# Performance work log

Hardware: AMD Instinct MI355X
Metric: run time of the kernel (lower is better)

## Reference

```python
import jax, jax.numpy as jnp
import numpy as np

B, N, D = 8, 2048, 512
S = 4096  # max_swaps


def setup_inputs() -> dict:
    key = jax.random.key(0)
    ks = jax.random.split(key, 5)
    h = jax.random.normal(ks[0], (B, N, D), dtype=jnp.float32)
    indices = jax.random.randint(ks[1], (B, S, 4), 0, N, dtype=jnp.int64)
    # MLP params (Linear stores weight as (out,in) in torch; we keep (in,out) and matmul)
    W1 = jax.random.normal(ks[2], (4 * D, D), dtype=jnp.float32) * (1.0 / np.sqrt(4 * D))
    b1 = jnp.zeros((D,), dtype=jnp.float32)
    W2 = jax.random.normal(ks[3], (D, D // 2), dtype=jnp.float32) * (1.0 / np.sqrt(D))
    b2 = jnp.zeros((D // 2,), dtype=jnp.float32)
    W3 = jax.random.normal(ks[4], (D // 2, 1), dtype=jnp.float32) * (1.0 / np.sqrt(D // 2))
    b3 = jnp.zeros((1,), dtype=jnp.float32)
    return {"h": h, "indices": indices, "W1": W1, "b1": b1, "W2": W2, "b2": b2, "W3": W3, "b3": b3}


def reference(h, indices, W1, b1, W2, b2, W3, b3):
    # h: (B, N, D); indices: (B, S, 4) node ids per swap
    swap_emb = jnp.take_along_axis(h[:, None, :, :], indices[..., None].astype(jnp.int32),
                                   axis=2)  # broadcast-gather -> (B, S, 4, D)
    # equivalently: h[batch_idx, indices]; implemented as per-batch gather
    swap_emb = jax.vmap(lambda hb, ib: hb[ib])(h, indices)  # (B, S, 4, D)
    swap_feats = swap_emb.reshape(h.shape[0], indices.shape[1], -1)  # (B, S, 4D)
    x = jax.nn.gelu(swap_feats @ W1 + b1, approximate=False)
    x = jax.nn.gelu(x @ W2 + b2, approximate=False)
    scores = (x @ W3 + b3)[..., 0]  # (B, S)
    rates = jax.nn.softplus(scores)
    return rates
```

## Files before the change

### kernel.cpp

```cpp
#include <hip/hip_runtime.h>
#include <math.h>

#define BATCH 8
#define NNODES 2048
#define DDIM 512
#define SWAPS 4096
#define M_TOTAL (BATCH * SWAPS)
#define KD DDIM
#define ND (4 * DDIM)
#define K2 DDIM
#define N2 (DDIM / 2)

typedef __attribute__((ext_vector_type(8))) __bf16 bf16x8;
typedef __attribute__((ext_vector_type(4))) float f32x4;
typedef __attribute__((ext_vector_type(8))) unsigned short us8;
typedef unsigned short ushort_t;

__device__ __forceinline__ float gelu_exact(float x) {
    return 0.5f * x * (1.0f + erff(x * 0.70710678118654752440f));
}
__device__ __forceinline__ float softplus_f(float x) {
    return fmaxf(x, 0.0f) + log1pf(expf(-fabsf(x)));
}
__device__ __forceinline__ unsigned short f2bf(float f) {
    unsigned int u = __builtin_bit_cast(unsigned int, f);
    u += 0x7FFFu + ((u >> 16) & 1u);
    return (unsigned short)(u >> 16);
}
__device__ __forceinline__ float bf2f(unsigned short s) {
    return __builtin_bit_cast(float, (unsigned int)s << 16);
}
__device__ __forceinline__ void glds16(const void* g, void* l) {
    __builtin_amdgcn_global_load_lds(
        (const __attribute__((address_space(1))) void*)g,
        (__attribute__((address_space(3))) void*)l, 16, 0, 0);
}

__global__ __launch_bounds__(256) void convert_kernel(
    const float* __restrict__ h, const float* __restrict__ W1,
    const float* __restrict__ W2, ushort_t* __restrict__ h_bf,
    ushort_t* __restrict__ W1pt, ushort_t* __restrict__ W2t)
{
    const int bid = blockIdx.x;
    if (bid < 8192) {
        size_t i = ((size_t)bid * 256 + threadIdx.x) * 4;
        float4 v = *(const float4*)(h + i);
        ushort4 o = { f2bf(v.x), f2bf(v.y), f2bf(v.z), f2bf(v.w) };
        *(ushort4*)(h_bf + i) = o;
    } else if (bid < 8192 + 1024) {
        size_t e = ((size_t)(bid - 8192) * 256 + threadIdx.x) * 4;
        const int k = (int)(e >> 9), n = (int)(e & 511);
        const int sg = k >> 9, d = k & 511;
        const int j = sg * 512 + n;
        float4 v = *(const float4*)(W1 + e);
        W1pt[(size_t)(j + 0) * KD + d] = f2bf(v.x);
        W1pt[(size_t)(j + 1) * KD + d] = f2bf(v.y);
        W1pt[(size_t)(j + 2) * KD + d] = f2bf(v.z);
        W1pt[(size_t)(j + 3) * KD + d] = f2bf(v.w);
    } else {
        size_t e = ((size_t)(bid - 9216) * 256 + threadIdx.x) * 4;
        const int k = (int)(e >> 8), n = (int)(e & 255);
        float4 v = *(const float4*)(W2 + e);
        W2t[(size_t)(n + 0) * K2 + k] = f2bf(v.x);
        W2t[(size_t)(n + 1) * K2 + k] = f2bf(v.y);
        W2t[(size_t)(n + 2) * K2 + k] = f2bf(v.z);
        W2t[(size_t)(n + 3) * K2 + k] = f2bf(v.w);
    }
}

__global__ __launch_bounds__(256) void gemm1_dense(
    const ushort_t* __restrict__ h_bf, const ushort_t* __restrict__ W1pt,
    ushort_t* __restrict__ P2)
{
    __shared__ __align__(16) char smem[32768];

    const int tid = threadIdx.x;
    const int w = tid >> 6, lane = tid & 63;
    const int quad = lane >> 4, l16 = lane & 15;
    const int wr = w >> 1, wc = w & 1;

    const int bid = blockIdx.x;
    const int xcd = bid & 7;
    const int r = bid >> 3;
    const int m0 = xcd * NNODES + (r & 15) * 128;
    const int n0 = (r >> 4) * 128;

    const int row0 = tid >> 2, sub = tid & 3;
    const int cg = (sub - (row0 >> 1)) & 3;
    const ushort_t* bA0 = h_bf + (size_t)(m0 + row0) * KD + cg * 8;
    const ushort_t* bA1 = h_bf + (size_t)(m0 + row0 + 64) * KD + cg * 8;
    const ushort_t* bB0 = W1pt + (size_t)(n0 + row0) * KD + cg * 8;
    const ushort_t* bB1 = W1pt + (size_t)(n0 + row0 + 64) * KD + cg * 8;

    int pa[4], pb[4];
    #pragma unroll
    for (int i = 0; i < 4; ++i) {
        const int rA = wr * 64 + i * 16 + l16;
        const int rB = wc * 64 + i * 16 + l16;
        pa[i] = rA * 64 + (((quad + (rA >> 1)) & 3) * 16);
        pb[i] = 8192 + rB * 64 + (((quad + (rB >> 1)) & 3) * 16);
    }

    f32x4 acc[4][4] = {};

    auto stage = [&](int kt, int half) {
        const int oo = kt * 32;
        char* base = smem + half * 16384;
        glds16(bA0 + oo, base + w * 1024);
        glds16(bA1 + oo, base + 4096 + w * 1024);
        glds16(bB0 + oo, base + 8192 + w * 1024);
        glds16(bB1 + oo, base + 12288 + w * 1024);
    };
    auto compute = [&](int half) {
        const char* base = smem + half * 16384;
        bf16x8 af[4], bfr[4];
        #pragma unroll
        for (int i = 0; i < 4; ++i) {
            af[i]  = *(const bf16x8*)(base + pa[i]);
            bfr[i] = *(const bf16x8*)(base + pb[i]);
        }
        #pragma unroll
        for (int i = 0; i < 4; ++i)
            #pragma unroll
            for (int jj = 0; jj < 4; ++jj)
                acc[i][jj] = __builtin_amdgcn_mfma_f32_16x16x32_bf16(
                    af[i], bfr[jj], acc[i][jj], 0, 0, 0);
    };

    for (int kt = 0; kt < 16; kt += 2) {
        stage(kt, 0);
        stage(kt + 1, 1);
        __syncthreads();
        compute(0);
        compute(1);
        __syncthreads();
    }

    #pragma unroll
    for (int jj = 0; jj < 4; ++jj) {
        const int j = n0 + wc * 64 + jj * 16 + l16;
        const int sg = j >> 9, nh = j & 511;
        const size_t base = ((size_t)(xcd * 2 + (nh >> 8)) * NNODES) * 1024
                          + (size_t)(sg << 8) + (nh & 255);
        #pragma unroll
        for (int i = 0; i < 4; ++i) {
            f32x4 v = acc[i][jj];
            #pragma unroll
            for (int rr = 0; rr < 4; ++rr) {
                const int node = (m0 + wr * 64 + i * 16 + quad * 4 + rr) & (NNODES - 1);
                P2[base + (size_t)node * 1024] = f2bf(v[rr]);
            }
        }
    }
}

__global__ __launch_bounds__(256) void gather_sum_kernel(
    const ushort_t* __restrict__ P2, const int* __restrict__ idx,
    const float* __restrict__ b1, ushort_t* __restrict__ x1_bf)
{
    const int bid = blockIdx.x;
    const int b = bid & 7;
    const int t = bid >> 3;
    const int nc = t >> 9;
    const int rg = t & 511;
    const int wave = threadIdx.x >> 6, lane = threadIdx.x & 63;
    const int rsel = lane >> 5, li = lane & 31;
    const int m = b * SWAPS + rg * 8 + wave * 2 + rsel;
    const int4 iv = *(const int4*)(idx + (size_t)m * 4);
    const ushort_t* Pr = P2 + ((size_t)(b * 2 + nc) * NNODES) * 1024;
    const int col = li * 8;

    float s[8];
    {
        const float* bp = b1 + nc * 256 + col;
        float4 ba = *(const float4*)bp;
        float4 bb = *(const float4*)(bp + 4);
        s[0] = ba.x; s[1] = ba.y; s[2] = ba.z; s[3] = ba.w;
        s[4] = bb.x; s[5] = bb.y; s[6] = bb.z; s[7] = bb.w;
    }
    const int nodes[4] = { iv.x, iv.y, iv.z, iv.w };
    #pragma unroll
    for (int sg = 0; sg < 4; ++sg) {
        us8 v = *(const us8*)(Pr + (size_t)nodes[sg] * 1024 + sg * 256 + col);
        #pragma unroll
        for (int u = 0; u < 8; ++u) s[u] += bf2f(v[u]);
    }
    us8 o;
    #pragma unroll
    for (int u = 0; u < 8; ++u)
        o[u] = f2bf(gelu_exact(s[u]));
    __builtin_nontemporal_store(o, (us8*)(x1_bf + (size_t)m * K2 + nc * 256 + col));
}

__global__ __launch_bounds__(256) void gemm2_partial(
    const ushort_t* __restrict__ x1_bf, const ushort_t* __restrict__ W2t,
    const float* __restrict__ b2, const float* __restrict__ W3,
    float* __restrict__ pp)
{
    __shared__ __align__(16) char smem[32768];

    const int tid = threadIdx.x;
    const int w = tid >> 6, lane = tid & 63;
    const int quad = lane >> 4, l16 = lane & 15;
    const int wr = w >> 1, wc = w & 1;
    const int m0 = blockIdx.y * 128, n0 = blockIdx.x * 128;

    const int row0 = tid >> 2, sub = tid & 3;
    const int cg = (sub - (row0 >> 1)) & 3;
    const ushort_t* bA0 = x1_bf + (size_t)(m0 + row0) * K2 + cg * 8;
    const ushort_t* bA1 = x1_bf + (size_t)(m0 + row0 + 64) * K2 + cg * 8;
    const ushort_t* bB0 = W2t + (size_t)(n0 + row0) * K2 + cg * 8;
    const ushort_t* bB1 = W2t + (size_t)(n0 + row0 + 64) * K2 + cg * 8;

    int pa[4], pb[4];
    #pragma unroll
    for (int i = 0; i < 4; ++i) {
        const int rA = wr * 64 + i * 16 + l16;
        const int rB = wc * 64 + i * 16 + l16;
        pa[i] = rA * 64 + (((quad + (rA >> 1)) & 3) * 16);
        pb[i] = 8192 + rB * 64 + (((quad + (rB >> 1)) & 3) * 16);
    }

    f32x4 acc[4][4] = {};

    auto stage = [&](int kt, int half) {
        const int oo = kt * 32;
        char* base = smem + half * 16384;
        glds16(bA0 + oo, base + w * 1024);
        glds16(bA1 + oo, base + 4096 + w * 1024);
        glds16(bB0 + oo, base + 8192 + w * 1024);
        glds16(bB1 + oo, base + 12288 + w * 1024);
    };
    auto compute = [&](int half) {
        const char* base = smem + half * 16384;
        bf16x8 af[4], bfr[4];
        #pragma unroll
        for (int i = 0; i < 4; ++i) {
            af[i]  = *(const bf16x8*)(base + pa[i]);
            bfr[i] = *(const bf16x8*)(base + pb[i]);
        }
        #pragma unroll
        for (int i = 0; i < 4; ++i)
            #pragma unroll
            for (int jj = 0; jj < 4; ++jj)
                acc[i][jj] = __builtin_amdgcn_mfma_f32_16x16x32_bf16(
                    af[i], bfr[jj], acc[i][jj], 0, 0, 0);
    };

    for (int kt = 0; kt < 16; kt += 2) {
        stage(kt, 0);
        stage(kt + 1, 1);
        __syncthreads();
        compute(0);
        compute(1);
        __syncthreads();
    }

    float w3r[4], b2r[4];
    #pragma unroll
    for (int jj = 0; jj < 4; ++jj) {
        const int n = n0 + wc * 64 + jj * 16 + l16;
        w3r[jj] = W3[n];
        b2r[jj] = b2[n];
    }
    float part[4][4];
    #pragma unroll
    for (int i = 0; i < 4; ++i)
        #pragma unroll
        for (int rr = 0; rr < 4; ++rr) part[i][rr] = 0.0f;
    #pragma unroll
    for (int i = 0; i < 4; ++i)
        #pragma unroll
        for (int jj = 0; jj < 4; ++jj) {
            f32x4 v = acc[i][jj];
            #pragma unroll
            for (int rr = 0; rr < 4; ++rr)
                part[i][rr] = fmaf(gelu_exact(v[rr] + b2r[jj]), w3r[jj], part[i][rr]);
        }
    #pragma unroll
    for (int off = 1; off < 16; off <<= 1)
        #pragma unroll
        for (int i = 0; i < 4; ++i)
            #pragma unroll
            for (int rr = 0; rr < 4; ++rr)
                part[i][rr] += __shfl_xor(part[i][rr], off);

    float* red = (float*)smem;
    __syncthreads();
    if (wc == 1 && l16 == 0) {
        #pragma unroll
        for (int i = 0; i < 4; ++i)
            #pragma unroll
            for (int rr = 0; rr < 4; ++rr)
                red[wr * 64 + i * 16 + quad * 4 + rr] = part[i][rr];
    }
    __syncthreads();
    if (wc == 0 && l16 == 0) {
        float* dst = pp + (size_t)blockIdx.x * M_TOTAL + m0;
        #pragma unroll
        for (int i = 0; i < 4; ++i)
            #pragma unroll
            for (int rr = 0; rr < 4; ++rr) {
                const int r2 = wr * 64 + i * 16 + quad * 4 + rr;
                dst[r2] = part[i][rr] + red[r2];
            }
    }
}

__global__ __launch_bounds__(256) void finalize_head(
    const float* __restrict__ pp, const float* __restrict__ b3,
    float* __restrict__ out)
{
    const int m = blockIdx.x * 256 + threadIdx.x;
    out[m] = softplus_f(pp[m] + pp[M_TOTAL + m] + b3[0]);
}

extern "C" void kernel_launch(void* const* d_in, const int* in_sizes, int n_in,
                              void* d_out, int out_size, void* d_ws, size_t ws_size,
                              hipStream_t stream) {
    const float* h   = (const float*)d_in[0];
    const int*   idx = (const int*)d_in[1];
    const float* W1  = (const float*)d_in[2];
    const float* b1  = (const float*)d_in[3];
    const float* W2  = (const float*)d_in[4];
    const float* b2  = (const float*)d_in[5];
    const float* W3  = (const float*)d_in[6];
    const float* b3  = (const float*)d_in[7];
    float* out = (float*)d_out;

    char* ws = (char*)d_ws;
    ushort_t* P2    = (ushort_t*)ws;
    float*    pp    = (float*)ws;
    ushort_t* h_bf  = (ushort_t*)(ws + (64u << 20));
    ushort_t* W1pt  = (ushort_t*)(ws + (80u << 20));
    ushort_t* x1_bf = (ushort_t*)(ws + (64u << 20));
    ushort_t* W2t   = (ushort_t*)(ws + (96u << 20));

    convert_kernel<<<9344, 256, 0, stream>>>(h, W1, W2, h_bf, W1pt, W2t);
    gemm1_dense<<<2048, 256, 0, stream>>>(h_bf, W1pt, P2);
    gather_sum_kernel<<<8192, 256, 0, stream>>>(P2, idx, b1, x1_bf);
    gemm2_partial<<<dim3(N2 / 128, M_TOTAL / 128), 256, 0, stream>>>(x1_bf, W2t, b2, W3, pp);
    finalize_head<<<M_TOTAL / 256, 256, 0, stream>>>(pp, b3, out);
}
```

Baseline: 202.6 us.

## Fuse gather-sum, GEMM2, head and softplus into one warp-specialized kernel

Replaces the gather_sum, gemm2_partial and finalize_head kernels with a single fused_tail kernel. Per block, half the waves gather P2 rows, add b1, apply GELU and write bf16 A tiles to LDS, while the other half load W2t tiles. Each block covers 64 rows and all 256 output columns, so the W3 dot product and softplus finish in-block. This removes the x1_bf and partial-score round trips through global memory and two launches. The cost is a grid of only 512 blocks, per-stage gather latency on the critical path, and W2 reloaded by every block.

```diff
diff --git a/kernel.cpp b/kernel.cpp
--- a/kernel.cpp
+++ b/kernel.cpp
@@ -7,7 +7,6 @@
 #define SWAPS 4096
 #define M_TOTAL (BATCH * SWAPS)
 #define KD DDIM
-#define ND (4 * DDIM)
 #define K2 DDIM
 #define N2 (DDIM / 2)
 
@@ -154,165 +153,129 @@
     }
 }
 
-__global__ __launch_bounds__(256) void gather_sum_kernel(
+__global__ __launch_bounds__(512) void fused_tail(
     const ushort_t* __restrict__ P2, const int* __restrict__ idx,
-    const float* __restrict__ b1, ushort_t* __restrict__ x1_bf)
+    const float* __restrict__ b1, const ushort_t* __restrict__ W2t,
+    const float* __restrict__ b2, const float* __restrict__ W3,
+    const float* __restrict__ b3, float* __restrict__ out)
 {
-    const int bid = blockIdx.x;
-    const int b = bid & 7;
-    const int t = bid >> 3;
-    const int nc = t >> 9;
-    const int rg = t & 511;
-    const int wave = threadIdx.x >> 6, lane = threadIdx.x & 63;
-    const int rsel = lane >> 5, li = lane & 31;
-    const int m = b * SWAPS + rg * 8 + wave * 2 + rsel;
-    const int4 iv = *(const int4*)(idx + (size_t)m * 4);
-    const ushort_t* Pr = P2 + ((size_t)(b * 2 + nc) * NNODES) * 1024;
-    const int col = li * 8;
-
-    float s[8];
-    {
-        const float* bp = b1 + nc * 256 + col;
-        float4 ba = *(const float4*)bp;
-        float4 bb = *(const float4*)(bp + 4);
-        s[0] = ba.x; s[1] = ba.y; s[2] = ba.z; s[3] = ba.w;
-        s[4] = bb.x; s[5] = bb.y; s[6] = bb.z; s[7] = bb.w;
-    }
-    const int nodes[4] = { iv.x, iv.y, iv.z, iv.w };
-    #pragma unroll
-    for (int sg = 0; sg < 4; ++sg) {
-        us8 v = *(const us8*)(Pr + (size_t)nodes[sg] * 1024 + sg * 256 + col);
-        #pragma unroll
-        for (int u = 0; u < 8; ++u) s[u] += bf2f(v[u]);
-    }
-    us8 o;
-    #pragma unroll
-    for (int u = 0; u < 8; ++u)
-        o[u] = f2bf(gelu_exact(s[u]));
-    __builtin_nontemporal_store(o, (us8*)(x1_bf + (size_t)m * K2 + nc * 256 + col));
-}
-
-__global__ __launch_bounds__(256) void gemm2_partial(
-    const ushort_t* __restrict__ x1_bf, const ushort_t* __restrict__ W2t,
-    const float* __restrict__ b2, const float* __restrict__ W3,
-    float* __restrict__ pp)
-{
-    __shared__ __align__(16) char smem[32768];
+    __shared__ __align__(16) char smem[40960];
 
     const int tid = threadIdx.x;
     const int w = tid >> 6, lane = tid & 63;
     const int quad = lane >> 4, l16 = lane & 15;
-    const int wr = w >> 1, wc = w & 1;
-    const int m0 = blockIdx.y * 128, n0 = blockIdx.x * 128;
-
-    const int row0 = tid >> 2, sub = tid & 3;
-    const int cg = (sub - (row0 >> 1)) & 3;
-    const ushort_t* bA0 = x1_bf + (size_t)(m0 + row0) * K2 + cg * 8;
-    const ushort_t* bA1 = x1_bf + (size_t)(m0 + row0 + 64) * K2 + cg * 8;
-    const ushort_t* bB0 = W2t + (size_t)(n0 + row0) * K2 + cg * 8;
-    const ushort_t* bB1 = W2t + (size_t)(n0 + row0 + 64) * K2 + cg * 8;
-
-    int pa[4], pb[4];
-    #pragma unroll
-    for (int i = 0; i < 4; ++i) {
-        const int rA = wr * 64 + i * 16 + l16;
-        const int rB = wc * 64 + i * 16 + l16;
-        pa[i] = rA * 64 + (((quad + (rA >> 1)) & 3) * 16);
-        pb[i] = 8192 + rB * 64 + (((quad + (rB >> 1)) & 3) * 16);
-    }
-
-    f32x4 acc[4][4] = {};
-
-    auto stage = [&](int kt, int half) {
-        const int oo = kt * 32;
-        char* base = smem + half * 16384;
-        glds16(bA0 + oo, base + w * 1024);
-        glds16(bA1 + oo, base + 4096 + w * 1024);
-        glds16(bB0 + oo, base + 8192 + w * 1024);
-        glds16(bB1 + oo, base + 12288 + w * 1024);
+    const int rf = w >> 1, hf = w & 1;
+
+    const int bid = blockIdx.x;
+    const int b = bid & 7;
+    const int m0 = b * SWAPS + (bid >> 3) * 64;
+
+    const int arow = tid >> 2;
+    const int ap = tid & 3;
+    const int acg = (ap - (arow >> 1)) & 3;
+    int4 iv = {0, 0, 0, 0};
+    if (tid < 256) iv = *(const int4*)(idx + (size_t)(m0 + arow) * 4);
+    const int nodes[4] = { iv.x, iv.y, iv.z, iv.w };
+    const ushort_t* P2b = P2 + (size_t)(b * 2) * NNODES * 1024;
+
+    const int vt = tid & 255;
+    const int brow0 = vt >> 2, bsub = vt & 3;
+    const int bcg = (bsub - (brow0 >> 1)) & 3;
+    const ushort_t* pB[4];
+    #pragma unroll
+    for (int g = 0; g < 4; ++g)
+        pB[g] = W2t + (size_t)(g * 64 + brow0) * K2 + bcg * 8;
+
+    const int rA = rf * 16 + l16;
+    const int paOff = rA * 64 + (((quad + (rA >> 1)) & 3) * 16);
+    int pb[8];
+    #pragma unroll
+    for (int jf = 0; jf < 8; ++jf) {
+        const int rB = hf * 128 + jf * 16 + l16;
+        pb[jf] = 4096 + rB * 64 + (((quad + (rB >> 1)) & 3) * 16);
+    }
+
+    f32x4 acc[8] = {};
+
+    auto stage = [&](int kc, int half) {
+        char* base = smem + half * 20480;
+        if (tid < 256) {
+            const int nc = kc >> 3;
+            const int pos0 = (kc & 7) * 32 + acg * 8;
+            const ushort_t* Pr = P2b + (size_t)nc * NNODES * 1024;
+            us8 v0 = *(const us8*)(Pr + (size_t)nodes[0] * 1024 + 0 * 256 + pos0);
+            us8 v1 = *(const us8*)(Pr + (size_t)nodes[1] * 1024 + 1 * 256 + pos0);
+            us8 v2 = *(const us8*)(Pr + (size_t)nodes[2] * 1024 + 2 * 256 + pos0);
+            us8 v3 = *(const us8*)(Pr + (size_t)nodes[3] * 1024 + 3 * 256 + pos0);
+            const float* bp = b1 + nc * 256 + pos0;
+            float4 ba = *(const float4*)bp;
+            float4 bb = *(const float4*)(bp + 4);
+            float s[8] = { ba.x, ba.y, ba.z, ba.w, bb.x, bb.y, bb.z, bb.w };
+            #pragma unroll
+            for (int e = 0; e < 8; ++e)
+                s[e] += bf2f(v0[e]) + bf2f(v1[e]) + bf2f(v2[e]) + bf2f(v3[e]);
+            us8 o;
+            #pragma unroll
+            for (int e = 0; e < 8; ++e) o[e] = f2bf(gelu_exact(s[e]));
+            *(us8*)(base + arow * 64 + ap * 16) = o;
+        } else {
+            const int oo = kc * 32;
+            char* bbase = base + 4096;
+            #pragma unroll
+            for (int g = 0; g < 4; ++g)
+                glds16(pB[g] + oo, bbase + g * 4096 + (w - 4) * 1024);
+        }
     };
     auto compute = [&](int half) {
-        const char* base = smem + half * 16384;
-        bf16x8 af[4], bfr[4];
-        #pragma unroll
-        for (int i = 0; i < 4; ++i) {
-            af[i]  = *(const bf16x8*)(base + pa[i]);
-            bfr[i] = *(const bf16x8*)(base + pb[i]);
-        }
-        #pragma unroll
-        for (int i = 0; i < 4; ++i)
-            #pragma unroll
-            for (int jj = 0; jj < 4; ++jj)
-                acc[i][jj] = __builtin_amdgcn_mfma_f32_16x16x32_bf16(
-                    af[i], bfr[jj], acc[i][jj], 0, 0, 0);
+        const char* base = smem + half * 20480;
+        bf16x8 af = *(const bf16x8*)(base + paOff);
+        #pragma unroll
+        for (int jf = 0; jf < 8; ++jf) {
+            bf16x8 bfr = *(const bf16x8*)(base + pb[jf]);
+            acc[jf] = __builtin_amdgcn_mfma_f32_16x16x32_bf16(af, bfr, acc[jf], 0, 0, 0);
+        }
     };
 
-    for (int kt = 0; kt < 16; kt += 2) {
-        stage(kt, 0);
-        stage(kt + 1, 1);
+    stage(0, 0);
+    __syncthreads();
+    for (int kc = 0; kc < 16; ++kc) {
+        if (kc < 15) stage(kc + 1, (kc + 1) & 1);
+        compute(kc & 1);
         __syncthreads();
-        compute(0);
-        compute(1);
-        __syncthreads();
-    }
-
-    float w3r[4], b2r[4];
-    #pragma unroll
-    for (int jj = 0; jj < 4; ++jj) {
-        const int n = n0 + wc * 64 + jj * 16 + l16;
-        w3r[jj] = W3[n];
-        b2r[jj] = b2[n];
-    }
-    float part[4][4];
-    #pragma unroll
-    for (int i = 0; i < 4; ++i)
-        #pragma unroll
-        for (int rr = 0; rr < 4; ++rr) part[i][rr] = 0.0f;
-    #pragma unroll
-    for (int i = 0; i < 4; ++i)
-        #pragma unroll
-        for (int jj = 0; jj < 4; ++jj) {
-            f32x4 v = acc[i][jj];
-            #pragma unroll
-            for (int rr = 0; rr < 4; ++rr)
-                part[i][rr] = fmaf(gelu_exact(v[rr] + b2r[jj]), w3r[jj], part[i][rr]);
-        }
+    }
+
+    float part[4] = {0.0f, 0.0f, 0.0f, 0.0f};
+    #pragma unroll
+    for (int jf = 0; jf < 8; ++jf) {
+        const int n = hf * 128 + jf * 16 + l16;
+        const float w3 = W3[n];
+        const float bb2 = b2[n];
+        f32x4 v = acc[jf];
+        #pragma unroll
+        for (int rr = 0; rr < 4; ++rr)
+            part[rr] = fmaf(gelu_exact(v[rr] + bb2), w3, part[rr]);
+    }
     #pragma unroll
     for (int off = 1; off < 16; off <<= 1)
         #pragma unroll
-        for (int i = 0; i < 4; ++i)
-            #pragma unroll
-            for (int rr = 0; rr < 4; ++rr)
-                part[i][rr] += __shfl_xor(part[i][rr], off);
+        for (int rr = 0; rr < 4; ++rr)
+            part[rr] += __shfl_xor(part[rr], off);
 
     float* red = (float*)smem;
+    if (hf == 1 && l16 == 0) {
+        #pragma unroll
+        for (int rr = 0; rr < 4; ++rr)
+            red[rf * 16 + quad * 4 + rr] = part[rr];
+    }
     __syncthreads();
-    if (wc == 1 && l16 == 0) {
-        #pragma unroll
-        for (int i = 0; i < 4; ++i)
-            #pragma unroll
-            for (int rr = 0; rr < 4; ++rr)
-                red[wr * 64 + i * 16 + quad * 4 + rr] = part[i][rr];
-    }
-    __syncthreads();
-    if (wc == 0 && l16 == 0) {
-        float* dst = pp + (size_t)blockIdx.x * M_TOTAL + m0;
-        #pragma unroll
-        for (int i = 0; i < 4; ++i)
-            #pragma unroll
-            for (int rr = 0; rr < 4; ++rr) {
-                const int r2 = wr * 64 + i * 16 + quad * 4 + rr;
-                dst[r2] = part[i][rr] + red[r2];
-            }
-    }
-}
-
-__global__ __launch_bounds__(256) void finalize_head(
-    const float* __restrict__ pp, const float* __restrict__ b3,
-    float* __restrict__ out)
-{
-    const int m = blockIdx.x * 256 + threadIdx.x;
-    out[m] = softplus_f(pp[m] + pp[M_TOTAL + m] + b3[0]);
+    if (hf == 0 && l16 == 0) {
+        const float bias3 = b3[0];
+        #pragma unroll
+        for (int rr = 0; rr < 4; ++rr) {
+            const int r2 = rf * 16 + quad * 4 + rr;
+            out[m0 + r2] = softplus_f(part[rr] + red[r2] + bias3);
+        }
+    }
 }
 
 extern "C" void kernel_launch(void* const* d_in, const int* in_sizes, int n_in,
@@ -330,15 +293,11 @@
 
     char* ws = (char*)d_ws;
     ushort_t* P2    = (ushort_t*)ws;
-    float*    pp    = (float*)ws;
     ushort_t* h_bf  = (ushort_t*)(ws + (64u << 20));
     ushort_t* W1pt  = (ushort_t*)(ws + (80u << 20));
-    ushort_t* x1_bf = (ushort_t*)(ws + (64u << 20));
     ushort_t* W2t   = (ushort_t*)(ws + (96u << 20));
 
     convert_kernel<<<9344, 256, 0, stream>>>(h, W1, W2, h_bf, W1pt, W2t);
     gemm1_dense<<<2048, 256, 0, stream>>>(h_bf, W1pt, P2);
-    gather_sum_kernel<<<8192, 256, 0, stream>>>(P2, idx, b1, x1_bf);
-    gemm2_partial<<<dim3(N2 / 128, M_TOTAL / 128), 256, 0, stream>>>(x1_bf, W2t, b2, W3, pp);
-    finalize_head<<<M_TOTAL / 256, 256, 0, stream>>>(pp, b3, out);
-}
+    fused_tail<<<512, 512, 0, stream>>>(P2, idx, b1, W2t, b2, W3, b3, out);
+}
```

After: 189.0 us. -6.7%, faster.
